# Optimization experiments

Measured on AMD Instinct MI355X. Metric: run time of the kernel, lower is better.

Reference implementation:

```python
import jax, jax.numpy as jnp
import numpy as np

GROUP = 64      # SVDQuant hard-coded group size
QMAX = 7.0      # symmetric int4: values in [-8, 7], scale = max|x| / 7
EPS = 1e-8


def setup_inputs() -> dict:
    key = jax.random.key(0)
    k0, k1, k2, k3, k4 = jax.random.split(key, 5)
    T, K, N, R = 4096, 4096, 4096, 32  # tokens, in_features, out_features, rank

    x = jax.random.normal(k0, (T, K), jnp.float32)

    # Full-precision weight, decomposed offline into low-rank + int4 residual
    w = jax.random.normal(k1, (N, K), jnp.float32) * 0.02
    proj_down = jax.random.normal(k2, (K, R), jnp.float32) * 0.02  # x @ proj_down -> [T, R]
    proj_up = jax.random.normal(k3, (R, N), jnp.float32) * 0.02    # [T, R] @ proj_up -> [T, N]
    residual = w - (proj_down @ proj_up).T  # [N, K]

    # Symmetric per-group int4 quantization of the residual weight
    rg = residual.reshape(N, K // GROUP, GROUP)
    wscales = jnp.maximum(jnp.max(jnp.abs(rg), axis=-1) / QMAX, EPS)  # [N, K/G]
    q_w = jnp.clip(jnp.round(rg / wscales[..., None]), -8, 7).astype(jnp.int8).reshape(N, K)

    smooth = jnp.ones((K,), jnp.float32)  # load_from_replicated sets smooth to ones
    bias = jax.random.normal(k4, (N,), jnp.float32) * 0.02
    return {
        "x": x,
        "q_w": q_w,
        "wscales": wscales,
        "proj_down": proj_down,
        "proj_up": proj_up,
        "smooth": smooth,
        "bias": bias,
    }


def reference(x, q_w, wscales, proj_down, proj_up, smooth, bias):
    T, K = x.shape
    N = q_w.shape[0]

    # smoothing (identity here, per load_from_replicated)
    xs = x * smooth

    # low-rank SVD correction branch (full precision)
    lr = (xs @ proj_down) @ proj_up  # [T, N]

    # W4A4 branch: symmetric per-token per-group int4 activation quantization
    xg = xs.reshape(T, K // GROUP, GROUP)
    ascales = jnp.maximum(jnp.max(jnp.abs(xg), axis=-1) / QMAX, EPS)  # [T, K/G]
    q_x = jnp.clip(jnp.round(xg / ascales[..., None]), -8.0, 7.0)
    x_dq = (q_x * ascales[..., None]).reshape(T, K)  # dequantized activations

    # dequantize int4 weights with per-(out_channel, group) scales
    w_dq = (q_w.astype(jnp.float32).reshape(N, K // GROUP, GROUP)
            * wscales[..., None]).reshape(N, K)

    # fused dequant-matmul + low-rank add + bias
    return lr + x_dq @ w_dq.T + bias
```

## Files before the change

### kernel.cpp

```cpp
#include <hip/hip_runtime.h>
#include <hip/hip_bf16.h>
#include <stdint.h>

#define Tdim 4096
#define Ndim 4096
#define Kdim 4096
#define K2   4160
#define NSPLIT 16
#define NT   130

using f32x4  = __attribute__((ext_vector_type(4))) float;
using bf16x8 = __attribute__((ext_vector_type(8))) short;

__device__ inline ushort f2bf(float f) {
  union { float f; unsigned u; } v; v.f = f;
  unsigned lsb = (v.u >> 16) & 1u;
  v.u += 0x7fffu + lsb;
  return (ushort)(v.u >> 16);
}

__device__ inline unsigned pack2(float a, float b) {
  return (unsigned)f2bf(a) | ((unsigned)f2bf(b) << 16);
}

__device__ inline float qd(float v, float s) {
  return fminf(fmaxf(rintf(v / s), -8.f), 7.f) * s;
}

__device__ inline void async16(const void* g, void* l) {
  __builtin_amdgcn_global_load_lds(
      (const __attribute__((address_space(1))) unsigned int*)g,
      (__attribute__((address_space(3))) unsigned int*)l, 16, 0, 0);
}

__global__ __launch_bounds__(256) void prep_pdT_kernel(
    const float* __restrict__ pd, ushort* __restrict__ pdT) {
  const int idx = blockIdx.x * 256 + threadIdx.x;
  const int n = idx >> 12;
  const int k = idx & 4095;
  pdT[(size_t)n * Kdim + k] = f2bf(pd[(size_t)k * 32 + n]);
}

__global__ __launch_bounds__(256) void prep_a_kernel(
    const float* __restrict__ x, const float* __restrict__ smooth,
    const ushort* __restrict__ pdT, ushort* __restrict__ A,
    float* __restrict__ partials) {
  __shared__ __attribute__((aligned(16))) ushort sXS[128 * 136];
  __shared__ __attribute__((aligned(16))) ushort sQ[128 * 136];
  const int tid  = threadIdx.x;
  const int lane = tid & 63;
  const int wave = tid >> 6;
  const int fr  = lane & 15;
  const int fkq = lane >> 4;
  const int fk  = fkq * 8;
  const int tok0 = blockIdx.x * 128;
  const int kc0  = blockIdx.y * 256;
  const int r = tid >> 1;
  const int g = tid & 1;
  const int srow2 = tid >> 2;
  const int scol2 = (tid & 3) * 8;

  f32x4 acc[2][2] = {};

  for (int c = 0; c < 2; ++c) {
    const int kbase = kc0 + c * 128;
    const int kcol  = g * 64;
    const float4* xp = (const float4*)&x[(size_t)(tok0 + r) * Kdim + kbase + kcol];
    const float4* sp = (const float4*)&smooth[kbase + kcol];
    float4 v[16];
#pragma unroll
    for (int q = 0; q < 16; ++q) {
      float4 xv = xp[q], sm = sp[q];
      v[q].x = xv.x * sm.x; v[q].y = xv.y * sm.y;
      v[q].z = xv.z * sm.z; v[q].w = xv.w * sm.w;
    }
    float a = 0.f;
#pragma unroll
    for (int q = 0; q < 16; ++q)
      a = fmaxf(a, fmaxf(fmaxf(fabsf(v[q].x), fabsf(v[q].y)),
                         fmaxf(fabsf(v[q].z), fabsf(v[q].w))));
    const float s = fmaxf(a / 7.0f, 1e-8f);
#pragma unroll
    for (int q2 = 0; q2 < 8; ++q2) {
      const float4 v0 = v[2 * q2], v1 = v[2 * q2 + 1];
      uint4 wx, wq;
      wx.x = pack2(v0.x, v0.y);           wx.y = pack2(v0.z, v0.w);
      wx.z = pack2(v1.x, v1.y);           wx.w = pack2(v1.z, v1.w);
      wq.x = pack2(qd(v0.x, s), qd(v0.y, s)); wq.y = pack2(qd(v0.z, s), qd(v0.w, s));
      wq.z = pack2(qd(v1.x, s), qd(v1.y, s)); wq.w = pack2(qd(v1.z, s), qd(v1.w, s));
      *(uint4*)&sXS[r * 136 + kcol + q2 * 8] = wx;
      *(uint4*)&sQ [r * 136 + kcol + q2 * 8] = wq;
    }
    __syncthreads();

#pragma unroll
    for (int kk = 0; kk < 4; ++kk) {
      const int kglob = kbase + kk * 32 + fk;
      bf16x8 af0 = *(const bf16x8*)&sXS[(wave * 32 + fr) * 136 + kk * 32 + fk];
      bf16x8 af1 = *(const bf16x8*)&sXS[(wave * 32 + 16 + fr) * 136 + kk * 32 + fk];
      bf16x8 b0 = *(const bf16x8*)&pdT[(size_t)fr * Kdim + kglob];
      bf16x8 b1 = *(const bf16x8*)&pdT[(size_t)(16 + fr) * Kdim + kglob];
      acc[0][0] = __builtin_amdgcn_mfma_f32_16x16x32_bf16(af0, b0, acc[0][0], 0, 0, 0);
      acc[0][1] = __builtin_amdgcn_mfma_f32_16x16x32_bf16(af0, b1, acc[0][1], 0, 0, 0);
      acc[1][0] = __builtin_amdgcn_mfma_f32_16x16x32_bf16(af1, b0, acc[1][0], 0, 0, 0);
      acc[1][1] = __builtin_amdgcn_mfma_f32_16x16x32_bf16(af1, b1, acc[1][1], 0, 0, 0);
    }

#pragma unroll
    for (int h = 0; h < 2; ++h) {
      const int rr = srow2 + h * 64;
#pragma unroll
      for (int u = 0; u < 4; ++u)
        *(uint4*)&A[(size_t)(tok0 + rr) * K2 + kbase + scol2 + u * 32] =
            *(const uint4*)&sQ[rr * 136 + scol2 + u * 32];
    }
    __syncthreads();
  }

  float* P = partials + (size_t)blockIdx.y * Tdim * 32;
#pragma unroll
  for (int i = 0; i < 2; ++i) {
    const int row0 = tok0 + wave * 32 + i * 16 + fkq * 4;
#pragma unroll
    for (int j = 0; j < 2; ++j) {
      const int col = j * 16 + fr;
#pragma unroll
      for (int rr = 0; rr < 4; ++rr)
        P[(size_t)(row0 + rr) * 32 + col] = acc[i][j][rr];
    }
  }
}

__global__ __launch_bounds__(256) void wprep_kernel(
    const int* __restrict__ qw, const float* __restrict__ wsc,
    const float* __restrict__ partials, const float* __restrict__ pu,
    ushort* __restrict__ A, ushort* __restrict__ B) {
  const int bid = blockIdx.x;
  if (bid < 8192) {
    const size_t idx = ((size_t)bid * 256 + threadIdx.x) * 8;
    const int n = (int)(idx >> 12);
    const int k = (int)(idx & 4095);
    const float s = wsc[n * 64 + (k >> 6)];
    const int4 q0 = *(const int4*)(qw + idx);
    const int4 q1 = *(const int4*)(qw + idx + 4);
    uint4 o;
    o.x = pack2((float)q0.x * s, (float)q0.y * s);
    o.y = pack2((float)q0.z * s, (float)q0.w * s);
    o.z = pack2((float)q1.x * s, (float)q1.y * s);
    o.w = pack2((float)q1.z * s, (float)q1.w * s);
    *(uint4*)(B + (size_t)n * K2 + k) = o;
  } else if (bid < 8192 + 1024) {
    const int idx = (bid - 8192) * 256 + threadIdx.x;
    const int token = idx >> 6, c = idx & 63;
    ushort v = 0;
    if (c < 32) {
      float s = 0.f;
#pragma unroll
      for (int p = 0; p < NSPLIT; ++p)
        s += partials[(size_t)p * Tdim * 32 + (size_t)token * 32 + c];
      v = f2bf(s);
    }
    A[(size_t)token * K2 + Kdim + c] = v;
  } else {
    const int idx = (bid - 9216) * 256 + threadIdx.x;
    const int n = idx >> 6, c = idx & 63;
    ushort v = 0;
    if (c < 32) v = f2bf(pu[(size_t)c * Ndim + n]);
    B[(size_t)n * K2 + Kdim + c] = v;
  }
}

__global__ __launch_bounds__(512, 2) void gemm_kernel(
    const ushort* __restrict__ A, const ushort* __restrict__ B,
    const float* __restrict__ bias, float* __restrict__ C) {
  __shared__ __attribute__((aligned(16))) ushort sA[3 * 8192];
  __shared__ __attribute__((aligned(16))) ushort sB[3 * 8192];
  const int tid  = threadIdx.x;
  const int lane = tid & 63;
  const int wave = tid >> 6;
  const int wm = wave >> 2;
  const int wn = wave & 3;
  const int fr  = lane & 15;
  const int fkq = lane >> 4;
  const int fchunk = (fkq ^ ((fr >> 1) & 3)) * 8;

  const int bid  = blockIdx.x;
  const int xcd  = bid & 7;
  const int i0   = bid >> 3;
  const int brow = (xcd >> 1) * 4 + (i0 >> 3);
  const int bcol = (xcd & 1) * 8 + (i0 & 7);
  const size_t arow0 = (size_t)brow * 256;
  const size_t brow0 = (size_t)bcol * 256;

  const int srow = tid >> 2;
  const int swz  = ((tid & 3) ^ ((tid >> 3) & 3)) * 8;
  const ushort* gA = A + (arow0 + srow) * K2 + swz;
  const ushort* gB = B + (brow0 + srow) * K2 + swz;

  const int rbase = wm * 128;
  const int cbase = wn * 64;

  f32x4 acc[8][4] = {};

#define MF(i, j, a, b) \
  acc[i][j] = __builtin_amdgcn_mfma_f32_16x16x32_bf16(a, b, acc[i][j], 0, 0, 0)
#define STAGE_A(st, so) \
  { async16(gA + (size_t)(st) * 32,                    &sA[(so) + tid * 8]);         \
    async16(gA + (size_t)(st) * 32 + (size_t)128 * K2, &sA[(so) + (tid + 512) * 8]); }
#define STAGE_B(st, so) \
  { async16(gB + (size_t)(st) * 32,                    &sB[(so) + tid * 8]);         \
    async16(gB + (size_t)(st) * 32 + (size_t)128 * K2, &sB[(so) + (tid + 512) * 8]); }
#define FENCE() asm volatile("" ::: "memory")
#define BARRIER() { FENCE(); __builtin_amdgcn_s_barrier(); FENCE(); }

  STAGE_A(0, 0); STAGE_B(0, 0);
  STAGE_A(1, 8192); STAGE_B(1, 8192);
  asm volatile("s_waitcnt vmcnt(4)" ::: "memory");
  BARRIER();

  for (int s = 0; s < NT; ++s) {
    const int sl  = (s % 3) * 8192;
    const int sn  = s + 2;
    const int sln = (sn % 3) * 8192;
    const ushort* al = &sA[sl];
    const ushort* bl = &sB[sl];

    bf16x8 af0 = *(const bf16x8*)&al[(rbase +  0 + fr) * 32 + fchunk];
    bf16x8 af1 = *(const bf16x8*)&al[(rbase + 16 + fr) * 32 + fchunk];
    bf16x8 af2 = *(const bf16x8*)&al[(rbase + 32 + fr) * 32 + fchunk];
    bf16x8 af3 = *(const bf16x8*)&al[(rbase + 48 + fr) * 32 + fchunk];
    bf16x8 bf0 = *(const bf16x8*)&bl[(cbase +  0 + fr) * 32 + fchunk];
    bf16x8 bf1 = *(const bf16x8*)&bl[(cbase + 16 + fr) * 32 + fchunk];
    bf16x8 bf2 = *(const bf16x8*)&bl[(cbase + 32 + fr) * 32 + fchunk];
    bf16x8 bf3 = *(const bf16x8*)&bl[(cbase + 48 + fr) * 32 + fchunk];

    if (sn < NT) { STAGE_A(sn, sln); STAGE_B(sn, sln); }

    bf16x8 ag0 = *(const bf16x8*)&al[(rbase +  64 + fr) * 32 + fchunk];
    bf16x8 ag1 = *(const bf16x8*)&al[(rbase +  80 + fr) * 32 + fchunk];
    bf16x8 ag2 = *(const bf16x8*)&al[(rbase +  96 + fr) * 32 + fchunk];
    bf16x8 ag3 = *(const bf16x8*)&al[(rbase + 112 + fr) * 32 + fchunk];
    __builtin_amdgcn_sched_barrier(0);

    __builtin_amdgcn_s_setprio(1);
    MF(0, 0, af0, bf0); MF(1, 0, af1, bf0); MF(2, 0, af2, bf0); MF(3, 0, af3, bf0);
    MF(0, 1, af0, bf1); MF(1, 1, af1, bf1); MF(2, 1, af2, bf1); MF(3, 1, af3, bf1);
    MF(0, 2, af0, bf2); MF(1, 2, af1, bf2); MF(2, 2, af2, bf2); MF(3, 2, af3, bf2);
    MF(0, 3, af0, bf3); MF(1, 3, af1, bf3); MF(2, 3, af2, bf3); MF(3, 3, af3, bf3);

    MF(4, 0, ag0, bf0); MF(5, 0, ag1, bf0); MF(6, 0, ag2, bf0); MF(7, 0, ag3, bf0);
    MF(4, 1, ag0, bf1); MF(5, 1, ag1, bf1); MF(6, 1, ag2, bf1); MF(7, 1, ag3, bf1);
    MF(4, 2, ag0, bf2); MF(5, 2, ag1, bf2); MF(6, 2, ag2, bf2); MF(7, 2, ag3, bf2);
    MF(4, 3, ag0, bf3); MF(5, 3, ag1, bf3); MF(6, 3, ag2, bf3); MF(7, 3, ag3, bf3);
    __builtin_amdgcn_s_setprio(0);

    if (s < NT - 2)       asm volatile("s_waitcnt vmcnt(4)" ::: "memory");
    else if (s == NT - 2) asm volatile("s_waitcnt vmcnt(0)" ::: "memory");
    BARRIER();
  }
#undef MF
#undef STAGE_A
#undef STAGE_B
#undef FENCE
#undef BARRIER

#pragma unroll
  for (int j = 0; j < 4; ++j) {
    const size_t col = brow0 + cbase + j * 16 + fr;
    const float bv = bias[col];
#pragma unroll
    for (int i = 0; i < 8; ++i) {
      const size_t row = arow0 + rbase + i * 16 + fkq * 4;
#pragma unroll
      for (int r = 0; r < 4; ++r)
        C[(row + r) * Ndim + col] = acc[i][j][r] + bv;
    }
  }
}

extern "C" void kernel_launch(void* const* d_in, const int* in_sizes, int n_in,
                              void* d_out, int out_size, void* d_ws, size_t ws_size,
                              hipStream_t stream) {
  const float* x      = (const float*)d_in[0];
  const int*   qw     = (const int*)d_in[1];
  const float* wsc    = (const float*)d_in[2];
  const float* pd     = (const float*)d_in[3];
  const float* pu     = (const float*)d_in[4];
  const float* smooth = (const float*)d_in[5];
  const float* bias   = (const float*)d_in[6];
  float* out = (float*)d_out;

  const size_t abytes = (size_t)Tdim * K2 * 2;
  ushort* A    = (ushort*)d_ws;
  ushort* B    = (ushort*)((char*)d_ws + abytes);
  ushort* pdT  = (ushort*)((char*)d_ws + 2 * abytes);
  float*  part = (float*)((char*)d_ws + 2 * abytes + 262144);

  hipLaunchKernelGGL(prep_pdT_kernel, dim3(512),    dim3(256), 0, stream, pd, pdT);
  hipLaunchKernelGGL(prep_a_kernel,   dim3(32, NSPLIT), dim3(256), 0, stream, x, smooth, pdT, A, part);
  hipLaunchKernelGGL(wprep_kernel,    dim3(10240),  dim3(256), 0, stream, qw, wsc, part, pu, A, B);
  hipLaunchKernelGGL(gemm_kernel,     dim3(256),    dim3(512), 0, stream, A, B, bias, out);
}
```

Measured before the change: 353.0 us.

## Restructure GEMM mainloop to 64-wide K tiles with double buffering and quadrant MFMA phases

The bf16 GEMM mainloop moves from 32-wide K tiles with a three-stage LDS ring to 64-wide K tiles with two LDS buffers, halving the iteration count. The LDS swizzle is widened to 8 chunks to suit the 64-element rows. Each iteration is split into four MFMA quadrants with LDS fragment loads interleaved between them and guarded by barriers, in a ping-pong style schedule. The aim is to cut per-iteration barrier and loop overhead and overlap LDS reads with MFMA work. In exchange there are many more barriers per tile and only one tile of global prefetch depth, with a full vmcnt(0) wait each iteration.

```diff
diff --git a/kernel.cpp b/kernel.cpp
--- a/kernel.cpp
+++ b/kernel.cpp
@@ -7,7 +7,7 @@
 #define Kdim 4096
 #define K2   4160
 #define NSPLIT 16
-#define NT   130
+#define NT64 65
 
 using f32x4  = __attribute__((ext_vector_type(4))) float;
 using bf16x8 = __attribute__((ext_vector_type(8))) short;
@@ -173,8 +173,8 @@
 __global__ __launch_bounds__(512, 2) void gemm_kernel(
     const ushort* __restrict__ A, const ushort* __restrict__ B,
     const float* __restrict__ bias, float* __restrict__ C) {
-  __shared__ __attribute__((aligned(16))) ushort sA[3 * 8192];
-  __shared__ __attribute__((aligned(16))) ushort sB[3 * 8192];
+  __shared__ __attribute__((aligned(16))) ushort sA[2 * 16384];
+  __shared__ __attribute__((aligned(16))) ushort sB[2 * 16384];
   const int tid  = threadIdx.x;
   const int lane = tid & 63;
   const int wave = tid >> 6;
@@ -182,7 +182,8 @@
   const int wn = wave & 3;
   const int fr  = lane & 15;
   const int fkq = lane >> 4;
-  const int fchunk = (fkq ^ ((fr >> 1) & 3)) * 8;
+  const int c0 = ((fkq    ) ^ (fr & 7)) * 8;
+  const int c1 = ((fkq + 4) ^ (fr & 7)) * 8;
 
   const int bid  = blockIdx.x;
   const int xcd  = bid & 7;
@@ -192,78 +193,103 @@
   const size_t arow0 = (size_t)brow * 256;
   const size_t brow0 = (size_t)bcol * 256;
 
-  const int srow = tid >> 2;
-  const int swz  = ((tid & 3) ^ ((tid >> 3) & 3)) * 8;
+  const int srow = tid >> 3;
+  const int swz  = ((tid & 7) ^ (srow & 7)) * 8;
   const ushort* gA = A + (arow0 + srow) * K2 + swz;
   const ushort* gB = B + (brow0 + srow) * K2 + swz;
 
+  f32x4 acc[8][4] = {};
+
+#define STAGE8(T)                                                            \
+  do {                                                                       \
+    const size_t tk = (size_t)(T) * 64;                                      \
+    const int so = (((T) & 1) * 16384) + tid * 8;                            \
+    async16(gA + tk,                     &sA[so]);                           \
+    async16(gA + tk + (size_t)64  * K2,  &sA[so + 4096]);                    \
+    async16(gA + tk + (size_t)128 * K2,  &sA[so + 8192]);                    \
+    async16(gA + tk + (size_t)192 * K2,  &sA[so + 12288]);                   \
+    async16(gB + tk,                     &sB[so]);                           \
+    async16(gB + tk + (size_t)64  * K2,  &sB[so + 4096]);                    \
+    async16(gB + tk + (size_t)128 * K2,  &sB[so + 8192]);                    \
+    async16(gB + tk + (size_t)192 * K2,  &sB[so + 12288]);                   \
+  } while (0)
+#define LDA(DST, ROFF)                                                       \
+  do {                                                                       \
+    _Pragma("unroll") for (int ii = 0; ii < 4; ++ii) {                       \
+      DST[ii][0] = *(const bf16x8*)&an[((ROFF) + ii * 16) * 64 + c0];        \
+      DST[ii][1] = *(const bf16x8*)&an[((ROFF) + ii * 16) * 64 + c1];        \
+    }                                                                        \
+  } while (0)
+#define LDB(DST, ROFF)                                                       \
+  do {                                                                       \
+    _Pragma("unroll") for (int jj = 0; jj < 2; ++jj) {                       \
+      DST[jj][0] = *(const bf16x8*)&bn[((ROFF) + jj * 16) * 64 + c0];        \
+      DST[jj][1] = *(const bf16x8*)&bn[((ROFF) + jj * 16) * 64 + c1];        \
+    }                                                                        \
+  } while (0)
+#define MFMA16(RB, CB, AF, BF)                                               \
+  do {                                                                       \
+    __builtin_amdgcn_s_setprio(1);                                           \
+    _Pragma("unroll") for (int kk = 0; kk < 2; ++kk)                         \
+      _Pragma("unroll") for (int jj = 0; jj < 2; ++jj)                       \
+        _Pragma("unroll") for (int ii = 0; ii < 4; ++ii)                     \
+          acc[(RB) + ii][(CB) + jj] =                                        \
+              __builtin_amdgcn_mfma_f32_16x16x32_bf16(                       \
+                  AF[ii][kk], BF[jj][kk], acc[(RB) + ii][(CB) + jj], 0, 0, 0); \
+    __builtin_amdgcn_s_setprio(0);                                           \
+  } while (0)
+#define FENCE() asm volatile("" ::: "memory")
+#define BARRIER() { FENCE(); __builtin_amdgcn_s_barrier(); FENCE(); }
+#define LGKM0()                                                              \
+  { asm volatile("s_waitcnt lgkmcnt(0)" ::: "memory");                       \
+    __builtin_amdgcn_sched_barrier(0); }
+
+  STAGE8(0);
+  asm volatile("s_waitcnt vmcnt(0)" ::: "memory");
+  BARRIER();
+
+  for (int t = 0; t < NT64; ++t) {
+    const int sl = (t & 1) * 16384;
+    const ushort* an = &sA[sl + (wm * 128 + fr) * 64];
+    const ushort* bn = &sB[sl + (wn * 64 + fr) * 64];
+    bf16x8 A0f[4][2], A1f[4][2], B0f[2][2], B1f[2][2];
+
+    LDA(A0f, 0);
+    LDB(B0f, 0);
+    if (t + 1 < NT64) STAGE8(t + 1);
+    asm volatile("s_waitcnt lgkmcnt(8)" ::: "memory");
+    __builtin_amdgcn_sched_barrier(0);
+    BARRIER();
+    LGKM0();
+    MFMA16(0, 0, A0f, B0f);
+    BARRIER();
+
+    LDA(A1f, 64);
+    BARRIER();
+    LGKM0();
+    MFMA16(4, 0, A1f, B0f);
+    BARRIER();
+
+    LDB(B1f, 32);
+    BARRIER();
+    LGKM0();
+    MFMA16(4, 2, A1f, B1f);
+    BARRIER();
+
+    MFMA16(0, 2, A0f, B1f);
+    if (t + 1 < NT64) asm volatile("s_waitcnt vmcnt(0)" ::: "memory");
+    BARRIER();
+  }
+#undef STAGE8
+#undef LDA
+#undef LDB
+#undef MFMA16
+#undef FENCE
+#undef BARRIER
+#undef LGKM0
+
   const int rbase = wm * 128;
   const int cbase = wn * 64;
-
-  f32x4 acc[8][4] = {};
-
-#define MF(i, j, a, b) \
-  acc[i][j] = __builtin_amdgcn_mfma_f32_16x16x32_bf16(a, b, acc[i][j], 0, 0, 0)
-#define STAGE_A(st, so) \
-  { async16(gA + (size_t)(st) * 32,                    &sA[(so) + tid * 8]);         \
-    async16(gA + (size_t)(st) * 32 + (size_t)128 * K2, &sA[(so) + (tid + 512) * 8]); }
-#define STAGE_B(st, so) \
-  { async16(gB + (size_t)(st) * 32,                    &sB[(so) + tid * 8]);         \
-    async16(gB + (size_t)(st) * 32 + (size_t)128 * K2, &sB[(so) + (tid + 512) * 8]); }
-#define FENCE() asm volatile("" ::: "memory")
-#define BARRIER() { FENCE(); __builtin_amdgcn_s_barrier(); FENCE(); }
-
-  STAGE_A(0, 0); STAGE_B(0, 0);
-  STAGE_A(1, 8192); STAGE_B(1, 8192);
-  asm volatile("s_waitcnt vmcnt(4)" ::: "memory");
-  BARRIER();
-
-  for (int s = 0; s < NT; ++s) {
-    const int sl  = (s % 3) * 8192;
-    const int sn  = s + 2;
-    const int sln = (sn % 3) * 8192;
-    const ushort* al = &sA[sl];
-    const ushort* bl = &sB[sl];
-
-    bf16x8 af0 = *(const bf16x8*)&al[(rbase +  0 + fr) * 32 + fchunk];
-    bf16x8 af1 = *(const bf16x8*)&al[(rbase + 16 + fr) * 32 + fchunk];
-    bf16x8 af2 = *(const bf16x8*)&al[(rbase + 32 + fr) * 32 + fchunk];
-    bf16x8 af3 = *(const bf16x8*)&al[(rbase + 48 + fr) * 32 + fchunk];
-    bf16x8 bf0 = *(const bf16x8*)&bl[(cbase +  0 + fr) * 32 + fchunk];
-    bf16x8 bf1 = *(const bf16x8*)&bl[(cbase + 16 + fr) * 32 + fchunk];
-    bf16x8 bf2 = *(const bf16x8*)&bl[(cbase + 32 + fr) * 32 + fchunk];
-    bf16x8 bf3 = *(const bf16x8*)&bl[(cbase + 48 + fr) * 32 + fchunk];
-
-    if (sn < NT) { STAGE_A(sn, sln); STAGE_B(sn, sln); }
-
-    bf16x8 ag0 = *(const bf16x8*)&al[(rbase +  64 + fr) * 32 + fchunk];
-    bf16x8 ag1 = *(const bf16x8*)&al[(rbase +  80 + fr) * 32 + fchunk];
-    bf16x8 ag2 = *(const bf16x8*)&al[(rbase +  96 + fr) * 32 + fchunk];
-    bf16x8 ag3 = *(const bf16x8*)&al[(rbase + 112 + fr) * 32 + fchunk];
-    __builtin_amdgcn_sched_barrier(0);
-
-    __builtin_amdgcn_s_setprio(1);
-    MF(0, 0, af0, bf0); MF(1, 0, af1, bf0); MF(2, 0, af2, bf0); MF(3, 0, af3, bf0);
-    MF(0, 1, af0, bf1); MF(1, 1, af1, bf1); MF(2, 1, af2, bf1); MF(3, 1, af3, bf1);
-    MF(0, 2, af0, bf2); MF(1, 2, af1, bf2); MF(2, 2, af2, bf2); MF(3, 2, af3, bf2);
-    MF(0, 3, af0, bf3); MF(1, 3, af1, bf3); MF(2, 3, af2, bf3); MF(3, 3, af3, bf3);
-
-    MF(4, 0, ag0, bf0); MF(5, 0, ag1, bf0); MF(6, 0, ag2, bf0); MF(7, 0, ag3, bf0);
-    MF(4, 1, ag0, bf1); MF(5, 1, ag1, bf1); MF(6, 1, ag2, bf1); MF(7, 1, ag3, bf1);
-    MF(4, 2, ag0, bf2); MF(5, 2, ag1, bf2); MF(6, 2, ag2, bf2); MF(7, 2, ag3, bf2);
-    MF(4, 3, ag0, bf3); MF(5, 3, ag1, bf3); MF(6, 3, ag2, bf3); MF(7, 3, ag3, bf3);
-    __builtin_amdgcn_s_setprio(0);
-
-    if (s < NT - 2)       asm volatile("s_waitcnt vmcnt(4)" ::: "memory");
-    else if (s == NT - 2) asm volatile("s_waitcnt vmcnt(0)" ::: "memory");
-    BARRIER();
-  }
-#undef MF
-#undef STAGE_A
-#undef STAGE_B
-#undef FENCE
-#undef BARRIER
-
 #pragma unroll
   for (int j = 0; j < 4; ++j) {
     const size_t col = brow0 + cbase + j * 16 + fr;
```

New measurement: 336.2 us. -4.7%, faster.

## Split GEMM main loop into two barrier phases with register-prefetched LDS fragments

Applied to the files above, without the earlier changes.

Restructures the bf16 MFMA main loop into two half-steps per K tile. Each half-step issues the LDS fragment reads for the next half while the current MFMAs run, using ping-pong B register buffers, with a barrier after each phase. It also changes the global-load swizzle term to be derived from the staging row, so the write pattern matches the read swizzle. The aim is to hide LDS read latency behind MFMA work, at the cost of twice as many barriers and more live registers.

```diff
diff --git a/kernel.cpp b/kernel.cpp
--- a/kernel.cpp
+++ b/kernel.cpp
@@ -193,7 +193,7 @@
   const size_t brow0 = (size_t)bcol * 256;
 
   const int srow = tid >> 2;
-  const int swz  = ((tid & 3) ^ ((tid >> 3) & 3)) * 8;
+  const int swz  = ((tid & 3) ^ ((srow >> 1) & 3)) * 8;
   const ushort* gA = A + (arow0 + srow) * K2 + swz;
   const ushort* gB = B + (brow0 + srow) * K2 + swz;
 
@@ -201,68 +201,82 @@
   const int cbase = wn * 64;
 
   f32x4 acc[8][4] = {};
-
-#define MF(i, j, a, b) \
-  acc[i][j] = __builtin_amdgcn_mfma_f32_16x16x32_bf16(a, b, acc[i][j], 0, 0, 0)
-#define STAGE_A(st, so) \
-  { async16(gA + (size_t)(st) * 32,                    &sA[(so) + tid * 8]);         \
-    async16(gA + (size_t)(st) * 32 + (size_t)128 * K2, &sA[(so) + (tid + 512) * 8]); }
-#define STAGE_B(st, so) \
-  { async16(gB + (size_t)(st) * 32,                    &sB[(so) + tid * 8]);         \
-    async16(gB + (size_t)(st) * 32 + (size_t)128 * K2, &sB[(so) + (tid + 512) * 8]); }
+  bf16x8 A03[4], A47[4], Bp[4], Bq[4];
+
+#define STAGE(S) do {                                                        \
+    const int so_ = ((S) % 3) * 8192;                                        \
+    const size_t gk_ = (size_t)(S) * 32;                                     \
+    async16(gA + gk_,                     &sA[so_ + tid * 8]);               \
+    async16(gA + gk_ + (size_t)128 * K2,  &sA[so_ + (tid + 512) * 8]);       \
+    async16(gB + gk_,                     &sB[so_ + tid * 8]);               \
+    async16(gB + gk_ + (size_t)128 * K2,  &sB[so_ + (tid + 512) * 8]);       \
+  } while (0)
 #define FENCE() asm volatile("" ::: "memory")
 #define BARRIER() { FENCE(); __builtin_amdgcn_s_barrier(); FENCE(); }
 
-  STAGE_A(0, 0); STAGE_B(0, 0);
-  STAGE_A(1, 8192); STAGE_B(1, 8192);
+#define PH1(S, BC, DOSTAGE, VMN) do {                                        \
+    const int sl_ = ((S) % 3) * 8192;                                        \
+    _Pragma("unroll") for (int ii = 0; ii < 4; ++ii)                         \
+      A47[ii] = *(const bf16x8*)&sA[sl_ + (rbase + 64 + ii * 16 + fr) * 32 + fchunk]; \
+    if (DOSTAGE) STAGE((S) + 2);                                             \
+    __builtin_amdgcn_sched_barrier(0);                                       \
+    __builtin_amdgcn_s_setprio(1);                                           \
+    _Pragma("unroll") for (int jj = 0; jj < 4; ++jj)                         \
+      _Pragma("unroll") for (int ii = 0; ii < 4; ++ii)                       \
+        acc[ii][jj] = __builtin_amdgcn_mfma_f32_16x16x32_bf16(               \
+            A03[ii], BC[jj], acc[ii][jj], 0, 0, 0);                          \
+    __builtin_amdgcn_s_setprio(0);                                           \
+    __builtin_amdgcn_sched_barrier(0);                                       \
+    asm volatile("s_waitcnt vmcnt(" #VMN ")" ::: "memory");                  \
+    BARRIER();                                                               \
+  } while (0)
+
+#define PH2(S, BC, BN, DOREAD) do {                                          \
+    if (DOREAD) {                                                            \
+      const int sl_ = (((S) + 1) % 3) * 8192;                                \
+      _Pragma("unroll") for (int ii = 0; ii < 4; ++ii)                       \
+        A03[ii] = *(const bf16x8*)&sA[sl_ + (rbase + ii * 16 + fr) * 32 + fchunk]; \
+      _Pragma("unroll") for (int jj = 0; jj < 4; ++jj)                       \
+        BN[jj] = *(const bf16x8*)&sB[sl_ + (cbase + jj * 16 + fr) * 32 + fchunk];  \
+    }                                                                        \
+    __builtin_amdgcn_sched_barrier(0);                                       \
+    __builtin_amdgcn_s_setprio(1);                                           \
+    _Pragma("unroll") for (int jj = 0; jj < 4; ++jj)                         \
+      _Pragma("unroll") for (int ii = 0; ii < 4; ++ii)                       \
+        acc[4 + ii][jj] = __builtin_amdgcn_mfma_f32_16x16x32_bf16(           \
+            A47[ii], BC[jj], acc[4 + ii][jj], 0, 0, 0);                      \
+    __builtin_amdgcn_s_setprio(0);                                           \
+    __builtin_amdgcn_sched_barrier(0);                                       \
+    BARRIER();                                                               \
+  } while (0)
+
+  STAGE(0);
+  STAGE(1);
   asm volatile("s_waitcnt vmcnt(4)" ::: "memory");
   BARRIER();
-
-  for (int s = 0; s < NT; ++s) {
-    const int sl  = (s % 3) * 8192;
-    const int sn  = s + 2;
-    const int sln = (sn % 3) * 8192;
-    const ushort* al = &sA[sl];
-    const ushort* bl = &sB[sl];
-
-    bf16x8 af0 = *(const bf16x8*)&al[(rbase +  0 + fr) * 32 + fchunk];
-    bf16x8 af1 = *(const bf16x8*)&al[(rbase + 16 + fr) * 32 + fchunk];
-    bf16x8 af2 = *(const bf16x8*)&al[(rbase + 32 + fr) * 32 + fchunk];
-    bf16x8 af3 = *(const bf16x8*)&al[(rbase + 48 + fr) * 32 + fchunk];
-    bf16x8 bf0 = *(const bf16x8*)&bl[(cbase +  0 + fr) * 32 + fchunk];
-    bf16x8 bf1 = *(const bf16x8*)&bl[(cbase + 16 + fr) * 32 + fchunk];
-    bf16x8 bf2 = *(const bf16x8*)&bl[(cbase + 32 + fr) * 32 + fchunk];
-    bf16x8 bf3 = *(const bf16x8*)&bl[(cbase + 48 + fr) * 32 + fchunk];
-
-    if (sn < NT) { STAGE_A(sn, sln); STAGE_B(sn, sln); }
-
-    bf16x8 ag0 = *(const bf16x8*)&al[(rbase +  64 + fr) * 32 + fchunk];
-    bf16x8 ag1 = *(const bf16x8*)&al[(rbase +  80 + fr) * 32 + fchunk];
-    bf16x8 ag2 = *(const bf16x8*)&al[(rbase +  96 + fr) * 32 + fchunk];
-    bf16x8 ag3 = *(const bf16x8*)&al[(rbase + 112 + fr) * 32 + fchunk];
-    __builtin_amdgcn_sched_barrier(0);
-
-    __builtin_amdgcn_s_setprio(1);
-    MF(0, 0, af0, bf0); MF(1, 0, af1, bf0); MF(2, 0, af2, bf0); MF(3, 0, af3, bf0);
-    MF(0, 1, af0, bf1); MF(1, 1, af1, bf1); MF(2, 1, af2, bf1); MF(3, 1, af3, bf1);
-    MF(0, 2, af0, bf2); MF(1, 2, af1, bf2); MF(2, 2, af2, bf2); MF(3, 2, af3, bf2);
-    MF(0, 3, af0, bf3); MF(1, 3, af1, bf3); MF(2, 3, af2, bf3); MF(3, 3, af3, bf3);
-
-    MF(4, 0, ag0, bf0); MF(5, 0, ag1, bf0); MF(6, 0, ag2, bf0); MF(7, 0, ag3, bf0);
-    MF(4, 1, ag0, bf1); MF(5, 1, ag1, bf1); MF(6, 1, ag2, bf1); MF(7, 1, ag3, bf1);
-    MF(4, 2, ag0, bf2); MF(5, 2, ag1, bf2); MF(6, 2, ag2, bf2); MF(7, 2, ag3, bf2);
-    MF(4, 3, ag0, bf3); MF(5, 3, ag1, bf3); MF(6, 3, ag2, bf3); MF(7, 3, ag3, bf3);
-    __builtin_amdgcn_s_setprio(0);
-
-    if (s < NT - 2)       asm volatile("s_waitcnt vmcnt(4)" ::: "memory");
-    else if (s == NT - 2) asm volatile("s_waitcnt vmcnt(0)" ::: "memory");
-    BARRIER();
-  }
-#undef MF
-#undef STAGE_A
-#undef STAGE_B
+#pragma unroll
+  for (int ii = 0; ii < 4; ++ii)
+    A03[ii] = *(const bf16x8*)&sA[(rbase + ii * 16 + fr) * 32 + fchunk];
+#pragma unroll
+  for (int jj = 0; jj < 4; ++jj)
+    Bp[jj] = *(const bf16x8*)&sB[(cbase + jj * 16 + fr) * 32 + fchunk];
+
+  for (int su = 0; su < 128; su += 2) {
+    PH1(su,     Bp, 1, 4);
+    PH2(su,     Bp, Bq, 1);
+    PH1(su + 1, Bq, 1, 4);
+    PH2(su + 1, Bq, Bp, 1);
+  }
+  PH1(128, Bp, 0, 0);
+  PH2(128, Bp, Bq, 1);
+  PH1(129, Bq, 0, 0);
+  PH2(129, Bq, Bp, 0);
+
+#undef STAGE
 #undef FENCE
 #undef BARRIER
+#undef PH1
+#undef PH2
 
 #pragma unroll
   for (int j = 0; j < 4; ++j) {
```

Result: faster. 336.1 us (-4.8%).
